# Optimization experiments

Hardware: AMD Instinct MI355X
Metric: run time of the kernel (lower is better)

The kernel has to match this reference:

```python
import jax, jax.numpy as jnp
import numpy as np

B, T, V, C, NB = 8, 2048, 1024, 128, 32


def setup_inputs() -> dict:
    key = jax.random.key(0)
    ks = jax.random.split(key, 6)
    x = jax.random.normal(ks[0], (B, T, V), jnp.float32)
    basis = jax.random.normal(ks[1], (V, 2 * NB), jnp.float32)
    q_coeffs = jax.random.normal(ks[2], (C, 2 * NB), jnp.float32) * 0.02
    k_coeffs = jax.random.normal(ks[3], (C, 2 * NB), jnp.float32) * 0.02
    v_coeffs = jax.random.normal(ks[4], (C, 2 * NB), jnp.float32) * 0.02
    o_coeffs = jax.random.normal(ks[5], (C, 2 * NB), jnp.float32) * 0.02
    decay = jnp.float32(0.95)
    out_scale = jnp.float32(0.1)
    return {"x": x, "basis": basis, "q_coeffs": q_coeffs, "k_coeffs": k_coeffs,
            "v_coeffs": v_coeffs, "o_coeffs": o_coeffs, "decay": decay, "out_scale": out_scale}


def reference(x, basis, q_coeffs, k_coeffs, v_coeffs, o_coeffs, decay, out_scale):
    # Fourier-parameterized projections: (V, C); softmax over vocab dim for q/k/v
    q_w = jax.nn.softmax(basis @ q_coeffs.T, axis=0)
    k_w = jax.nn.softmax(basis @ k_coeffs.T, axis=0)
    v_w = jax.nn.softmax(basis @ v_coeffs.T, axis=0)
    o_w = basis @ o_coeffs.T  # (V, C), no softmax

    q = x @ q_w  # (B, T, C)
    k = x @ k_w
    v = x @ v_w
    d = jax.nn.sigmoid(decay)

    M0 = jnp.zeros((x.shape[0], q_w.shape[1], q_w.shape[1]), x.dtype)  # (B, C, C)

    def step(M, qkv_t):
        q_t, k_t, v_t = qkv_t  # each (B, C)
        retrieved = jnp.einsum('bc,bcd->bd', q_t, M)  # read BEFORE write (as in torch loop)
        M_new = d * M + jnp.einsum('bc,bd->bcd', k_t, v_t)
        return M_new, retrieved

    qT = jnp.swapaxes(q, 0, 1)  # (T, B, C)
    kT = jnp.swapaxes(k, 0, 1)
    vT = jnp.swapaxes(v, 0, 1)
    _, rs = jax.lax.scan(step, M0, (qT, kT, vT))  # rs: (T, B, C)
    retrieved = jnp.swapaxes(rs, 0, 1)  # (B, T, C)
    return (retrieved @ o_w.T) * out_scale  # (B, T, V)
```

## Files before the change

kernel.cpp:

```cpp
#include <hip/hip_runtime.h>
#include <math.h>

#define B_   8
#define T_   2048
#define V_   1024
#define C_   128
#define NB2  64
#define L_   32
#define NC_  64

typedef _Float16 f16_t;
typedef f16_t f16x8 __attribute__((ext_vector_type(8)));
typedef float f32x4 __attribute__((ext_vector_type(4)));

__device__ __forceinline__ float sigmoidf_(float x){ return 1.0f/(1.0f+expf(-x)); }

__device__ __forceinline__ void gload_lds16(const void* g, void* l){
  __builtin_amdgcn_global_load_lds(
      (const __attribute__((address_space(1))) uint32_t*)g,
      (__attribute__((address_space(3))) uint32_t*)l, 16, 0, 0);
}

__global__ __launch_bounds__(256) void weights_kernel(
    const float* __restrict__ basis,
    const float* __restrict__ qc, const float* __restrict__ kc,
    const float* __restrict__ vc, const float* __restrict__ oc,
    f16_t* __restrict__ Wo, f16_t* __restrict__ Wt)
{
  int blk  = blockIdx.x;
  int proj = blk >> 7;
  int c    = blk & 127;
  const float* coeffs = (proj==0)?qc : (proj==1)?kc : (proj==2)?vc : oc;

  __shared__ float coef[NB2];
  __shared__ float red[256];
  int tid = threadIdx.x;
  if (tid < NB2) coef[tid] = coeffs[c*NB2 + tid];
  __syncthreads();

  float l[4];
  for (int i=0;i<4;i++){
    int v = tid + i*256;
    const float4* bp = (const float4*)(basis + (size_t)v*NB2);
    float s = 0.f;
    #pragma unroll
    for (int f=0; f<NB2/4; f++){
      float4 b4 = bp[f];
      s += b4.x*coef[f*4+0] + b4.y*coef[f*4+1] + b4.z*coef[f*4+2] + b4.w*coef[f*4+3];
    }
    l[i] = s;
  }
  if (proj == 3){
    for (int i=0;i<4;i++){ int v = tid+i*256; Wo[(size_t)v*C_ + c] = (f16_t)l[i]; }
    return;
  }
  float mx = fmaxf(fmaxf(l[0],l[1]), fmaxf(l[2],l[3]));
  red[tid] = mx; __syncthreads();
  for (int s=128; s>0; s>>=1){ if (tid<s) red[tid] = fmaxf(red[tid], red[tid+s]); __syncthreads(); }
  mx = red[0]; __syncthreads();
  float sum = 0.f;
  for (int i=0;i<4;i++) sum += expf(l[i]-mx);
  red[tid] = sum; __syncthreads();
  for (int s=128; s>0; s>>=1){ if (tid<s) red[tid] += red[tid+s]; __syncthreads(); }
  float inv = 1.0f/red[0];
  f16_t* tp = Wt + ((size_t)proj*C_ + c)*V_;
  for (int i=0;i<4;i++){
    int v = tid+i*256;
    tp[v] = (f16_t)(expf(l[i]-mx)*inv);
  }
}

#define BM 64
#define BN 128
#define BK 64
#define PADK 72
#define NF_  384
#define NT_PROJ (V_/BK)

__global__ __launch_bounds__(512, 1) void proj_fused_kernel(
    const float* __restrict__ x,
    const f16_t* __restrict__ Wt,
    float* __restrict__ out)
{
  const int M = B_*T_;
  int m0 = blockIdx.x * BM;

  __shared__ __align__(16) f16_t As[BM][PADK];
  __shared__ __align__(16) f16_t Bsh[NF_*BK];

  int tid  = threadIdx.x;
  int lane = tid & 63;
  int w    = tid >> 6;
  int wm   = (w >> 2) * 32;
  int wn   = (w & 3) * 96;
  int lr   = lane & 15;
  int lg   = lane >> 4;

  const float* xbase = x + (size_t)m0*V_;

  f32x4 acc[2][6] = {};

  for (int kt = 0; kt < NT_PROJ; kt++){
    #pragma unroll
    for (int i=0;i<6;i++){
      int ci = i*512 + tid;
      int r  = ci >> 3, ch = ci & 7;
      const f16_t* src = Wt + (size_t)r*V_ + kt*BK + ((ch ^ (r&7))<<3);
      gload_lds16(src, &Bsh[ci*8]);
    }
    #pragma unroll
    for (int i=0;i<2;i++){
      int ci = i*512 + tid;
      int row = ci >> 4, q = ci & 15;
      float4 xv = *(const float4*)(xbase + (size_t)row*V_ + kt*BK + q*4);
      union { f16_t h[4]; ushort4 u; } hh;
      hh.h[0]=(f16_t)xv.x; hh.h[1]=(f16_t)xv.y; hh.h[2]=(f16_t)xv.z; hh.h[3]=(f16_t)xv.w;
      *(ushort4*)&As[row][q*4] = hh.u;
    }
    __syncthreads();

    #pragma unroll
    for (int kh=0; kh<2; kh++){
      f16x8 a[2];
      #pragma unroll
      for (int mt=0; mt<2; mt++)
        a[mt] = *(f16x8*)&As[wm + mt*16 + lr][kh*32 + lg*8];
      #pragma unroll
      for (int nt=0; nt<6; nt++){
        int n  = wn + nt*16 + lr;
        int c0 = kh*4 + lg;
        f16x8 b = *(f16x8*)&Bsh[n*BK + ((c0 ^ (n&7))<<3)];
        #pragma unroll
        for (int mt=0; mt<2; mt++)
          acc[mt][nt] = __builtin_amdgcn_mfma_f32_16x16x32_f16(a[mt], b, acc[mt][nt], 0,0,0);
      }
    }
    __syncthreads();
  }

  #pragma unroll
  for (int mt=0; mt<2; mt++)
    #pragma unroll
    for (int nt=0; nt<6; nt++){
      int n   = wn + nt*16 + lr;
      int p   = n >> 7;
      int col = n & 127;
      float* op = out + (size_t)p*M*C_;
      #pragma unroll
      for (int r=0; r<4; r++){
        int row = m0 + wm + mt*16 + lg*4 + r;
        op[(size_t)row*C_ + col] = acc[mt][nt][r];
      }
    }
}

__global__ __launch_bounds__(256) void kvsum_kernel(
    const float* __restrict__ k, const float* __restrict__ v,
    const float* __restrict__ dptr, float* __restrict__ kv)
{
  int ci = blockIdx.x, b = blockIdx.y;
  float d = sigmoidf_(dptr[0]);
  __shared__ float ks[L_][132];
  __shared__ float vs[L_][132];
  int tid = threadIdx.x;
  const float* kp = k + ((size_t)b*T_ + ci*L_)*C_;
  const float* vp = v + ((size_t)b*T_ + ci*L_)*C_;
  #pragma unroll
  for (int i=0;i<4;i++){
    int idx = tid + i*256;
    int j = idx >> 5, c4 = idx & 31;
    float w = powf(d, (float)(L_-1-j));
    float4 k4 = *(const float4*)(kp + (size_t)j*C_ + c4*4);
    k4.x*=w; k4.y*=w; k4.z*=w; k4.w*=w;
    *(float4*)&ks[j][c4*4] = k4;
    *(float4*)&vs[j][c4*4] = *(const float4*)(vp + (size_t)j*C_ + c4*4);
  }
  __syncthreads();
  int tc = tid >> 4, td = tid & 15;
  float acc[8][8] = {};
  for (int j=0;j<L_;j++){
    float kr[8], vr[8];
    *(float4*)&kr[0] = *(float4*)&ks[j][tc*8];
    *(float4*)&kr[4] = *(float4*)&ks[j][tc*8+4];
    *(float4*)&vr[0] = *(float4*)&vs[j][td*8];
    *(float4*)&vr[4] = *(float4*)&vs[j][td*8+4];
    #pragma unroll
    for (int a=0;a<8;a++)
      #pragma unroll
      for (int bb=0;bb<8;bb++) acc[a][bb] += kr[a]*vr[bb];
  }
  float* op = kv + ((size_t)b*NC_ + ci)*C_*C_;
  for (int a=0;a<8;a++)
    for (int b4=0;b4<2;b4++)
      *(float4*)(op + (size_t)(tc*8+a)*C_ + td*8 + b4*4) =
        make_float4(acc[a][b4*4],acc[a][b4*4+1],acc[a][b4*4+2],acc[a][b4*4+3]);
}

__global__ __launch_bounds__(256) void scan_kernel(
    float* __restrict__ kv, const float* __restrict__ dptr)
{
  int idx = blockIdx.x*256 + threadIdx.x;
  int b = idx >> 14, e = idx & 16383;
  float d  = sigmoidf_(dptr[0]);
  float dL = powf(d, (float)L_);
  float* p = kv + (size_t)b*NC_*C_*C_ + e;
  float m = 0.f;
  for (int i=0;i<NC_;i++){
    float s = p[(size_t)i*C_*C_];
    p[(size_t)i*C_*C_] = m;
    m = dL*m + s;
  }
}

__global__ __launch_bounds__(256, 4) void intra_kernel(
    const float* __restrict__ q, const float* __restrict__ k,
    const float* __restrict__ v, const float* __restrict__ Minit,
    const float* __restrict__ dptr,
    f16_t* __restrict__ ret)
{
  int ci = blockIdx.x, b = blockIdx.y;
  int tid = threadIdx.x;
  float d = sigmoidf_(dptr[0]);
  __shared__ float qs[L_][132];
  __shared__ float kvs[L_][132];
  __shared__ __align__(16) float Ms[2][L_][C_];
  __shared__ float ps[L_][33];
  __shared__ float dpow[L_+1];
  if (tid <= L_) dpow[tid] = powf(d, (float)tid);

  const float* qp = q + ((size_t)b*T_ + ci*L_)*C_;
  const float* kp = k + ((size_t)b*T_ + ci*L_)*C_;
  const float* vp = v + ((size_t)b*T_ + ci*L_)*C_;
  const float* Mp = Minit + ((size_t)b*NC_ + ci)*C_*C_;

  #pragma unroll
  for (int i=0;i<4;i++){
    int cidx = i*256 + tid;
    gload_lds16(Mp + (size_t)cidx*4, &Ms[0][0][cidx*4]);
  }
  #pragma unroll
  for (int i=0;i<4;i++){
    int idx = tid + i*256;
    int j = idx >> 5, c4 = idx & 31;
    *(float4*)&qs[j][c4*4]  = *(const float4*)(qp + (size_t)j*C_ + c4*4);
    *(float4*)&kvs[j][c4*4] = *(const float4*)(kp + (size_t)j*C_ + c4*4);
  }
  __syncthreads();

  #pragma unroll
  for (int i=0;i<4;i++){
    int cidx = i*256 + tid;
    gload_lds16(Mp + (size_t)L_*C_ + cidx*4, &Ms[1][0][cidx*4]);
  }

  {
    int tr = tid >> 4, tj = tid & 15;
    float s[2][2] = {};
    for (int c4=0;c4<32;c4++){
      float4 q4[2], k4[2];
      #pragma unroll
      for (int i=0;i<2;i++) q4[i] = *(float4*)&qs[tr*2+i][c4*4];
      #pragma unroll
      for (int i=0;i<2;i++) k4[i] = *(float4*)&kvs[tj*2+i][c4*4];
      #pragma unroll
      for (int a=0;a<2;a++)
        #pragma unroll
        for (int bb=0;bb<2;bb++)
          s[a][bb] += q4[a].x*k4[bb].x + q4[a].y*k4[bb].y + q4[a].z*k4[bb].z + q4[a].w*k4[bb].w;
    }
    #pragma unroll
    for (int a=0;a<2;a++)
      #pragma unroll
      for (int bb=0;bb<2;bb++){
        int r = tr*2+a, j = tj*2+bb;
        ps[r][j] = (j < r) ? s[a][bb]*dpow[r-1-j] : 0.f;
      }
  }
  __syncthreads();

  #pragma unroll
  for (int i=0;i<4;i++){
    int idx = tid + i*256;
    int j = idx >> 5, c4 = idx & 31;
    *(float4*)&kvs[j][c4*4] = *(const float4*)(vp + (size_t)j*C_ + c4*4);
  }

  int tx = tid & 31, ty = tid >> 5;
  float acc[4][4] = {};

#define INTRA_MCHUNK(buf, cc) do { \
    for (int c=0;c<L_;c++){ \
      float4 m4 = *(float4*)&Ms[buf][c][tx*4]; \
      _Pragma("unroll") \
      for (int r=0;r<4;r++){ \
        float qv = qs[ty*4+r][(cc)*L_ + c]; \
        acc[r][0] += qv*m4.x; acc[r][1] += qv*m4.y; \
        acc[r][2] += qv*m4.z; acc[r][3] += qv*m4.w; \
      } \
    } \
  } while(0)

  INTRA_MCHUNK(0, 0);
  __syncthreads();

  #pragma unroll
  for (int i=0;i<4;i++){
    int cidx = i*256 + tid;
    gload_lds16(Mp + (size_t)2*L_*C_ + cidx*4, &Ms[0][0][cidx*4]);
  }
  INTRA_MCHUNK(1, 1);
  __syncthreads();

  #pragma unroll
  for (int i=0;i<4;i++){
    int cidx = i*256 + tid;
    gload_lds16(Mp + (size_t)3*L_*C_ + cidx*4, &Ms[1][0][cidx*4]);
  }
  INTRA_MCHUNK(0, 2);
  __syncthreads();

  INTRA_MCHUNK(1, 3);
#undef INTRA_MCHUNK

  #pragma unroll
  for (int r=0;r<4;r++){
    float sc = dpow[ty*4+r];
    #pragma unroll
    for (int j=0;j<4;j++) acc[r][j] *= sc;
  }
  for (int j=0;j<L_;j++){
    float4 v4 = *(float4*)&kvs[j][tx*4];
    #pragma unroll
    for (int r=0;r<4;r++){
      float p = ps[ty*4+r][j];
      acc[r][0] += p*v4.x; acc[r][1] += p*v4.y; acc[r][2] += p*v4.z; acc[r][3] += p*v4.w;
    }
  }
  size_t rbase = ((size_t)b*T_ + ci*L_)*C_;
  for (int r=0;r<4;r++){
    union { f16_t h[4]; ushort4 u; } hh;
    #pragma unroll
    for (int j=0;j<4;j++) hh.h[j] = (f16_t)acc[r][j];
    *(ushort4*)(ret + rbase + (size_t)(ty*4+r)*C_ + tx*4) = hh.u;
  }
}

__global__ __launch_bounds__(256, 2) void out_mfma_kernel(
    const f16_t* __restrict__ A, const f16_t* __restrict__ Bw,
    const float* __restrict__ scl, float* __restrict__ out)
{
  int m0 = blockIdx.x * BM;
  int n0 = blockIdx.y * BN;
  float osc = scl[0];

  __shared__ f16_t As[BM][PADK];
  __shared__ f16_t Bs[BN][PADK];

  int tid  = threadIdx.x;
  int lane = tid & 63;
  int w    = tid >> 6;
  int wm   = (w >> 1) * 32;
  int wn   = (w & 1) * 64;
  int lr   = lane & 15;
  int lg   = lane >> 4;

  f32x4 acc[2][4] = {};

  for (int kt = 0; kt < 2; kt++){
    #pragma unroll
    for (int i=0;i<2;i++){
      int ci = tid + i*256;
      int row = ci >> 3, ch = ci & 7;
      *(uint4*)&As[row][ch*8] = *(const uint4*)(A + (size_t)(m0+row)*C_ + kt*BK + ch*8);
    }
    #pragma unroll
    for (int i=0;i<4;i++){
      int ci = tid + i*256;
      int n = ci >> 3, ch = ci & 7;
      *(uint4*)&Bs[n][ch*8] = *(const uint4*)(Bw + (size_t)(n0+n)*C_ + kt*BK + ch*8);
    }
    __syncthreads();

    #pragma unroll
    for (int kh=0; kh<2; kh++){
      f16x8 a[2];
      #pragma unroll
      for (int mt=0; mt<2; mt++)
        a[mt] = *(f16x8*)&As[wm + mt*16 + lr][kh*32 + lg*8];
      #pragma unroll
      for (int nt=0; nt<4; nt++){
        f16x8 b = *(f16x8*)&Bs[wn + nt*16 + lr][kh*32 + lg*8];
        #pragma unroll
        for (int mt=0; mt<2; mt++)
          acc[mt][nt] = __builtin_amdgcn_mfma_f32_16x16x32_f16(a[mt], b, acc[mt][nt], 0,0,0);
      }
    }
    __syncthreads();
  }

  #pragma unroll
  for (int mt=0; mt<2; mt++)
    #pragma unroll
    for (int nt=0; nt<4; nt++)
      #pragma unroll
      for (int r=0; r<4; r++){
        int row = m0 + wm + mt*16 + lg*4 + r;
        int col = n0 + wn + nt*16 + lr;
        out[(size_t)row*V_ + col] = acc[mt][nt][r] * osc;
      }
}

extern "C" void kernel_launch(void* const* d_in, const int* in_sizes, int n_in,
                              void* d_out, int out_size, void* d_ws, size_t ws_size,
                              hipStream_t stream)
{
  const float* x     = (const float*)d_in[0];
  const float* basis = (const float*)d_in[1];
  const float* qc    = (const float*)d_in[2];
  const float* kc    = (const float*)d_in[3];
  const float* vc    = (const float*)d_in[4];
  const float* oc    = (const float*)d_in[5];
  const float* dptr  = (const float*)d_in[6];
  const float* sptr  = (const float*)d_in[7];
  float* out = (float*)d_out;
  float* ws  = (float*)d_ws;

  const size_t M = (size_t)B_*T_;
  f16_t* Wo  = (f16_t*)ws;
  f16_t* Wt  = (f16_t*)(ws + 65536);
  float* qkv = ws + 262144;
  f16_t* ret = (f16_t*)(ws + 6553600);
  float* kv  = ws + 7602176;

  float* q = qkv;
  float* k = qkv + M*C_;
  float* v = qkv + 2*M*C_;

  hipLaunchKernelGGL(weights_kernel, dim3(512), dim3(256), 0, stream,
                     basis, qc, kc, vc, oc, Wo, Wt);
  hipLaunchKernelGGL(proj_fused_kernel, dim3(256), dim3(512), 0, stream,
                     x, Wt, qkv);
  hipLaunchKernelGGL(kvsum_kernel, dim3(NC_, B_), dim3(256), 0, stream, k, v, dptr, kv);
  hipLaunchKernelGGL(scan_kernel, dim3(512), dim3(256), 0, stream, kv, dptr);
  hipLaunchKernelGGL(intra_kernel, dim3(NC_, B_), dim3(256), 0, stream,
                     q, k, v, kv, dptr, ret);
  hipLaunchKernelGGL(out_mfma_kernel, dim3(256, 8), dim3(256), 0, stream,
                     ret, Wo, sptr, out);
}
```

Baseline: 240.8 us.

## Split intra-chunk kernel over output column halves; drop LDS staging in output GEMM

The intra-chunk kernel now launches a third grid dimension that splits the 128 output columns into two halves. Each block loads only its half of the state matrix and V and computes 2 rows by 4 columns per thread. This doubles the block count from 512 to 1024 to fill the GPU better, at the cost of recomputing the QK^T score tile in both halves. The output MFMA kernel now reads A and B fragments straight from global memory instead of staging them in LDS, removing the shared memory and barriers. The risk is that those direct global fragment loads are uncoalesced and repeated across waves.

```diff
diff --git a/kernel.cpp b/kernel.cpp
--- a/kernel.cpp
+++ b/kernel.cpp
@@ -212,18 +212,18 @@
   }
 }
 
-__global__ __launch_bounds__(256, 4) void intra_kernel(
+__global__ __launch_bounds__(256) void intra_kernel(
     const float* __restrict__ q, const float* __restrict__ k,
     const float* __restrict__ v, const float* __restrict__ Minit,
     const float* __restrict__ dptr,
     f16_t* __restrict__ ret)
 {
-  int ci = blockIdx.x, b = blockIdx.y;
+  int ci = blockIdx.x, b = blockIdx.y, h = blockIdx.z;
   int tid = threadIdx.x;
   float d = sigmoidf_(dptr[0]);
-  __shared__ float qs[L_][132];
-  __shared__ float kvs[L_][132];
-  __shared__ __align__(16) float Ms[2][L_][C_];
+  __shared__ float qs[L_][130];
+  __shared__ float kvs[L_][130];
+  __shared__ __align__(16) float Ms[2][L_][64];
   __shared__ float ps[L_][33];
   __shared__ float dpow[L_+1];
   if (tid <= L_) dpow[tid] = powf(d, (float)tid);
@@ -231,12 +231,13 @@
   const float* qp = q + ((size_t)b*T_ + ci*L_)*C_;
   const float* kp = k + ((size_t)b*T_ + ci*L_)*C_;
   const float* vp = v + ((size_t)b*T_ + ci*L_)*C_;
-  const float* Mp = Minit + ((size_t)b*NC_ + ci)*C_*C_;
-
-  #pragma unroll
-  for (int i=0;i<4;i++){
+  const float* Mp = Minit + ((size_t)b*NC_ + ci)*C_*C_ + h*64;
+
+  #pragma unroll
+  for (int i=0;i<2;i++){
     int cidx = i*256 + tid;
-    gload_lds16(Mp + (size_t)cidx*4, &Ms[0][0][cidx*4]);
+    int r = cidx >> 4, c4 = cidx & 15;
+    gload_lds16(Mp + (size_t)r*C_ + c4*4, &Ms[0][0][0] + cidx*4);
   }
   #pragma unroll
   for (int i=0;i<4;i++){
@@ -248,9 +249,10 @@
   __syncthreads();
 
   #pragma unroll
-  for (int i=0;i<4;i++){
+  for (int i=0;i<2;i++){
     int cidx = i*256 + tid;
-    gload_lds16(Mp + (size_t)L_*C_ + cidx*4, &Ms[1][0][cidx*4]);
+    int r = cidx >> 4, c4 = cidx & 15;
+    gload_lds16(Mp + (size_t)(L_ + r)*C_ + c4*4, &Ms[1][0][0] + cidx*4);
   }
 
   {
@@ -279,21 +281,21 @@
   __syncthreads();
 
   #pragma unroll
-  for (int i=0;i<4;i++){
+  for (int i=0;i<2;i++){
     int idx = tid + i*256;
-    int j = idx >> 5, c4 = idx & 31;
-    *(float4*)&kvs[j][c4*4] = *(const float4*)(vp + (size_t)j*C_ + c4*4);
-  }
-
-  int tx = tid & 31, ty = tid >> 5;
-  float acc[4][4] = {};
+    int j = idx >> 4, c4 = idx & 15;
+    *(float4*)&kvs[j][c4*4] = *(const float4*)(vp + (size_t)j*C_ + h*64 + c4*4);
+  }
+
+  int tx = tid & 15, ty = tid >> 4;
+  float acc[2][4] = {};
 
 #define INTRA_MCHUNK(buf, cc) do { \
     for (int c=0;c<L_;c++){ \
       float4 m4 = *(float4*)&Ms[buf][c][tx*4]; \
       _Pragma("unroll") \
-      for (int r=0;r<4;r++){ \
-        float qv = qs[ty*4+r][(cc)*L_ + c]; \
+      for (int r=0;r<2;r++){ \
+        float qv = qs[ty*2+r][(cc)*L_ + c]; \
         acc[r][0] += qv*m4.x; acc[r][1] += qv*m4.y; \
         acc[r][2] += qv*m4.z; acc[r][3] += qv*m4.w; \
       } \
@@ -304,17 +306,19 @@
   __syncthreads();
 
   #pragma unroll
-  for (int i=0;i<4;i++){
+  for (int i=0;i<2;i++){
     int cidx = i*256 + tid;
-    gload_lds16(Mp + (size_t)2*L_*C_ + cidx*4, &Ms[0][0][cidx*4]);
+    int r = cidx >> 4, c4 = cidx & 15;
+    gload_lds16(Mp + (size_t)(2*L_ + r)*C_ + c4*4, &Ms[0][0][0] + cidx*4);
   }
   INTRA_MCHUNK(1, 1);
   __syncthreads();
 
   #pragma unroll
-  for (int i=0;i<4;i++){
+  for (int i=0;i<2;i++){
     int cidx = i*256 + tid;
-    gload_lds16(Mp + (size_t)3*L_*C_ + cidx*4, &Ms[1][0][cidx*4]);
+    int r = cidx >> 4, c4 = cidx & 15;
+    gload_lds16(Mp + (size_t)(3*L_ + r)*C_ + c4*4, &Ms[1][0][0] + cidx*4);
   }
   INTRA_MCHUNK(0, 2);
   __syncthreads();
@@ -323,38 +327,35 @@
 #undef INTRA_MCHUNK
 
   #pragma unroll
-  for (int r=0;r<4;r++){
-    float sc = dpow[ty*4+r];
+  for (int r=0;r<2;r++){
+    float sc = dpow[ty*2+r];
     #pragma unroll
     for (int j=0;j<4;j++) acc[r][j] *= sc;
   }
   for (int j=0;j<L_;j++){
     float4 v4 = *(float4*)&kvs[j][tx*4];
     #pragma unroll
-    for (int r=0;r<4;r++){
-      float p = ps[ty*4+r][j];
+    for (int r=0;r<2;r++){
+      float p = ps[ty*2+r][j];
       acc[r][0] += p*v4.x; acc[r][1] += p*v4.y; acc[r][2] += p*v4.z; acc[r][3] += p*v4.w;
     }
   }
-  size_t rbase = ((size_t)b*T_ + ci*L_)*C_;
-  for (int r=0;r<4;r++){
-    union { f16_t h[4]; ushort4 u; } hh;
-    #pragma unroll
-    for (int j=0;j<4;j++) hh.h[j] = (f16_t)acc[r][j];
-    *(ushort4*)(ret + rbase + (size_t)(ty*4+r)*C_ + tx*4) = hh.u;
-  }
-}
-
-__global__ __launch_bounds__(256, 2) void out_mfma_kernel(
+  size_t rbase = ((size_t)b*T_ + ci*L_)*C_ + h*64;
+  for (int r=0;r<2;r++){
+    union { f16_t h4[4]; ushort4 u; } hh;
+    #pragma unroll
+    for (int j=0;j<4;j++) hh.h4[j] = (f16_t)acc[r][j];
+    *(ushort4*)(ret + rbase + (size_t)(ty*2+r)*C_ + tx*4) = hh.u;
+  }
+}
+
+__global__ __launch_bounds__(256) void out_mfma_kernel(
     const f16_t* __restrict__ A, const f16_t* __restrict__ Bw,
     const float* __restrict__ scl, float* __restrict__ out)
 {
   int m0 = blockIdx.x * BM;
   int n0 = blockIdx.y * BN;
   float osc = scl[0];
-
-  __shared__ f16_t As[BM][PADK];
-  __shared__ f16_t Bs[BN][PADK];
 
   int tid  = threadIdx.x;
   int lane = tid & 63;
@@ -366,36 +367,19 @@
 
   f32x4 acc[2][4] = {};
 
-  for (int kt = 0; kt < 2; kt++){
-    #pragma unroll
-    for (int i=0;i<2;i++){
-      int ci = tid + i*256;
-      int row = ci >> 3, ch = ci & 7;
-      *(uint4*)&As[row][ch*8] = *(const uint4*)(A + (size_t)(m0+row)*C_ + kt*BK + ch*8);
-    }
-    #pragma unroll
-    for (int i=0;i<4;i++){
-      int ci = tid + i*256;
-      int n = ci >> 3, ch = ci & 7;
-      *(uint4*)&Bs[n][ch*8] = *(const uint4*)(Bw + (size_t)(n0+n)*C_ + kt*BK + ch*8);
-    }
-    __syncthreads();
-
-    #pragma unroll
-    for (int kh=0; kh<2; kh++){
-      f16x8 a[2];
+  #pragma unroll
+  for (int kh=0; kh<4; kh++){
+    f16x8 a[2];
+    #pragma unroll
+    for (int mt=0; mt<2; mt++)
+      a[mt] = *(const f16x8*)(A + (size_t)(m0 + wm + mt*16 + lr)*C_ + kh*32 + lg*8);
+    #pragma unroll
+    for (int nt=0; nt<4; nt++){
+      f16x8 bfr = *(const f16x8*)(Bw + (size_t)(n0 + wn + nt*16 + lr)*C_ + kh*32 + lg*8);
       #pragma unroll
       for (int mt=0; mt<2; mt++)
-        a[mt] = *(f16x8*)&As[wm + mt*16 + lr][kh*32 + lg*8];
-      #pragma unroll
-      for (int nt=0; nt<4; nt++){
-        f16x8 b = *(f16x8*)&Bs[wn + nt*16 + lr][kh*32 + lg*8];
-        #pragma unroll
-        for (int mt=0; mt<2; mt++)
-          acc[mt][nt] = __builtin_amdgcn_mfma_f32_16x16x32_f16(a[mt], b, acc[mt][nt], 0,0,0);
-      }
-    }
-    __syncthreads();
+        acc[mt][nt] = __builtin_amdgcn_mfma_f32_16x16x32_f16(a[mt], bfr, acc[mt][nt], 0,0,0);
+    }
   }
 
   #pragma unroll
@@ -442,7 +426,7 @@
                      x, Wt, qkv);
   hipLaunchKernelGGL(kvsum_kernel, dim3(NC_, B_), dim3(256), 0, stream, k, v, dptr, kv);
   hipLaunchKernelGGL(scan_kernel, dim3(512), dim3(256), 0, stream, kv, dptr);
-  hipLaunchKernelGGL(intra_kernel, dim3(NC_, B_), dim3(256), 0, stream,
+  hipLaunchKernelGGL(intra_kernel, dim3(NC_, B_, 2), dim3(256), 0, stream,
                      q, k, v, kv, dptr, ret);
   hipLaunchKernelGGL(out_mfma_kernel, dim3(256, 8), dim3(256), 0, stream,
                      ret, Wo, sptr, out);
```

Measured after the change: 275.4 us. +14.4%, slower.
